# Kernel tuning notes

Hardware: AMD Instinct MI355X
Metric: run time of the kernel (lower is better)

## Reference

```python
import jax, jax.numpy as jnp
import numpy as np

B, S, D, H, MEL = 64, 512, 512, 8, 80
HD = D // H  # head dim


def _lstm_cell(x, h, c, w_ih, w_hh, b_ih, b_hh):
    # torch gate order: i, f, g, o
    gates = x @ w_ih.T + h @ w_hh.T + b_ih + b_hh
    i, f, g, o = jnp.split(gates, 4, axis=-1)
    c = jax.nn.sigmoid(f) * c + jax.nn.sigmoid(i) * jnp.tanh(g)
    h = jax.nn.sigmoid(o) * jnp.tanh(c)
    return h, c


def setup_inputs() -> dict:
    key = jax.random.key(0)
    ks = jax.random.split(key, 24)
    s = 0.05
    inp = {"encoder_output": jax.random.normal(ks[0], (B, S, D), jnp.float32)}
    # MultiheadAttention params (torch layout: in_proj [3D, D])
    inp["attn_in_w"] = jax.random.normal(ks[1], (3 * D, D), jnp.float32) * s
    inp["attn_in_b"] = jax.random.normal(ks[2], (3 * D,), jnp.float32) * s
    inp["attn_out_w"] = jax.random.normal(ks[3], (D, D), jnp.float32) * s
    inp["attn_out_b"] = jax.random.normal(ks[4], (D,), jnp.float32) * s
    # LSTM1 (2 layers)
    names = [("l1_w_ih0", (4 * D, D)), ("l1_w_hh0", (4 * D, D)), ("l1_b_ih0", (4 * D,)), ("l1_b_hh0", (4 * D,)),
             ("l1_w_ih1", (4 * D, D)), ("l1_w_hh1", (4 * D, D)), ("l1_b_ih1", (4 * D,)), ("l1_b_hh1", (4 * D,)),
             ("l2_w_ih", (4 * D, D)), ("l2_w_hh", (4 * D, D)), ("l2_b_ih", (4 * D,)), ("l2_b_hh", (4 * D,)),
             ("proj_w", (MEL, D)), ("proj_b", (MEL,))]
    for i, (n, shp) in enumerate(names):
        inp[n] = jax.random.normal(ks[5 + i], shp, jnp.float32) * s
    return inp


def reference(encoder_output, attn_in_w, attn_in_b, attn_out_w, attn_out_b,
              l1_w_ih0, l1_w_hh0, l1_b_ih0, l1_b_hh0,
              l1_w_ih1, l1_w_hh1, l1_b_ih1, l1_b_hh1,
              l2_w_ih, l2_w_hh, l2_b_ih, l2_b_hh, proj_w, proj_b):
    b, s, d = encoder_output.shape
    max_len = s * 5
    wq, wk, wv = jnp.split(attn_in_w, 3, axis=0)
    bq, bk, bv = jnp.split(attn_in_b, 3, axis=0)
    # Precompute K, V over encoder output: [B, S, H, HD]
    K = (encoder_output @ wk.T + bk).reshape(b, s, H, HD)
    V = (encoder_output @ wv.T + bv).reshape(b, s, H, HD)
    scale = 1.0 / np.sqrt(HD)

    def attend(x):  # x: [B, D] single-token query
        q = ((x @ wq.T + bq) * scale).reshape(b, H, HD)
        scores = jnp.einsum('bhd,bshd->bhs', q, K)
        w = jax.nn.softmax(scores, axis=-1)
        ctx = jnp.einsum('bhs,bshd->bhd', w, V).reshape(b, d)
        return ctx @ attn_out_w.T + attn_out_b

    zeros = jnp.zeros((b, d), encoder_output.dtype)
    carry0 = (zeros, zeros, zeros, zeros, zeros, zeros, zeros)

    def step(carry, _):
        h10, c10, h11, c11, h2, c2, dec_in = carry
        h10, c10 = _lstm_cell(dec_in, h10, c10, l1_w_ih0, l1_w_hh0, l1_b_ih0, l1_b_hh0)
        h11, c11 = _lstm_cell(h10, h11, c11, l1_w_ih1, l1_w_hh1, l1_b_ih1, l1_b_hh1)
        attn_out = attend(h11)
        h2, c2 = _lstm_cell(attn_out, h2, c2, l2_w_ih, l2_w_hh, l2_b_ih, l2_b_hh)
        out = h2 @ proj_w.T + proj_b  # [B, MEL]
        return (h10, c10, h11, c11, h2, c2, h2), out

    _, ys = jax.lax.scan(step, carry0, None, length=max_len)
    return jnp.transpose(ys, (1, 0, 2))  # [B, max_len, MEL]
```

## Files before the change

kernel.cpp:

```cpp
#include <hip/hip_runtime.h>
#include <hip/hip_bf16.h>
#include <hip/hip_fp8.h>

#define DEV_INLINE __device__ __forceinline__

typedef __attribute__((ext_vector_type(8))) short bf16x8;
typedef __attribute__((ext_vector_type(4))) float f32x4;
typedef unsigned long long ull;

constexpr int Bc = 64, Sc = 512, Dc = 512, Hc = 8, HDc = 64, MELc = 80, Tc = 2560;
constexpr int OUTSTRIDE = Tc * MELc;

constexpr size_t SZ_KP8 = 64ull * 8 * 512 * 64;
constexpr size_t SZ_VP  = 64ull * 8 * 512 * 64 * 2;
constexpr size_t SZ_PL  = 128ull * 2048 * 16;
constexpr size_t OFF_KP8 = 0;
constexpr size_t OFF_VP  = OFF_KP8 + SZ_KP8;
constexpr size_t OFF_PL0 = OFF_VP + SZ_VP;
constexpr size_t OFF_PL1 = OFF_PL0 + SZ_PL;
constexpr size_t OFF_PL2 = OFF_PL1 + SZ_PL;
constexpr size_t OFF_PWQ = OFF_PL2 + SZ_PL;
constexpr size_t OFF_PP  = OFF_PWQ + 524288;
constexpr size_t OFF_BL0 = OFF_PP + 81920;
constexpr size_t OFF_BL1 = OFF_BL0 + 8192;
constexpr size_t OFF_BL2 = OFF_BL1 + 8192;
constexpr size_t OFF_B2E = OFF_BL2 + 8192;
constexpr size_t OFF_W2E = OFF_B2E + 8192;
constexpr size_t OFF_WOT = OFF_W2E + 2097152;
constexpr size_t OFF_ACT = OFF_WOT + 1048576;
constexpr size_t OFF_FLG = OFF_ACT + 524288;

constexpr unsigned DYN_LDS = 137344;

DEV_INLINE float bf2f(short s) { return __uint_as_float(((unsigned)(unsigned short)s) << 16); }
DEV_INLINE short f2bf(float f) { union { __hip_bfloat16 h; short s; } u; u.h = __float2bfloat16(f); return u.s; }
DEV_INLINE float sig_f(float x) { return 1.0f / (1.0f + __expf(-x)); }
DEV_INLINE float tanh_f(float x) {
  float ax = fabsf(x);
  float e = __expf(fminf(2.0f * ax, 80.0f));
  float r = 1.0f - 2.0f / (e + 1.0f);
  return copysignf(r, x);
}
DEV_INLINE bf16x8 cvt8(const float* p) {
  bf16x8 r;
#pragma unroll
  for (int i = 0; i < 8; ++i) r[i] = f2bf(p[i]);
  return r;
}
DEV_INLINE float fp8tof(unsigned v) {
  __hip_fp8_e4m3 t; t.__x = (__hip_fp8_storage_t)v; return (float)t;
}

DEV_INLINE ull ld_dev_u64(const void* p) {
  return __hip_atomic_load((const ull*)p, __ATOMIC_RELAXED, __HIP_MEMORY_SCOPE_AGENT);
}
DEV_INLINE void st_dev_u64(void* p, ull v) {
  __hip_atomic_store((ull*)p, v, __ATOMIC_RELAXED, __HIP_MEMORY_SCOPE_AGENT);
}
DEV_INLINE bf16x8 ld_frag(const __hip_bfloat16* p) {
  union { bf16x8 v; ull u[2]; } r;
  r.u[0] = ld_dev_u64(p);
  r.u[1] = ld_dev_u64((const char*)p + 8);
  return r.v;
}

__global__ __launch_bounds__(256) void gemm_setup(const float* __restrict__ A,
                                                  const float* __restrict__ Bt,
                                                  const float* __restrict__ bias,
                                                  __hip_bfloat16* __restrict__ dst,
                                                  unsigned char* __restrict__ dst8,
                                                  int mode) {
  int tid = threadIdx.x, lane = tid & 63, wv = tid >> 6;
  int m0 = blockIdx.y * 64 + wv * 16;
  int nb = blockIdx.x * 64;
  int mrow = m0 + (lane & 15);
  int kb = (lane >> 4) * 8;
  f32x4 acc0 = {0,0,0,0}, acc1 = {0,0,0,0}, acc2 = {0,0,0,0}, acc3 = {0,0,0,0};
  const float* arow = A + (size_t)mrow * 512 + kb;
  const float* b0r = Bt + (size_t)(nb + 0 * 16 + (lane & 15)) * 512 + kb;
  const float* b1r = Bt + (size_t)(nb + 1 * 16 + (lane & 15)) * 512 + kb;
  const float* b2r = Bt + (size_t)(nb + 2 * 16 + (lane & 15)) * 512 + kb;
  const float* b3r = Bt + (size_t)(nb + 3 * 16 + (lane & 15)) * 512 + kb;
  for (int kk = 0; kk < 16; ++kk) {
    bf16x8 af = cvt8(arow + kk * 32);
    acc0 = __builtin_amdgcn_mfma_f32_16x16x32_bf16(af, cvt8(b0r + kk * 32), acc0, 0, 0, 0);
    acc1 = __builtin_amdgcn_mfma_f32_16x16x32_bf16(af, cvt8(b1r + kk * 32), acc1, 0, 0, 0);
    acc2 = __builtin_amdgcn_mfma_f32_16x16x32_bf16(af, cvt8(b2r + kk * 32), acc2, 0, 0, 0);
    acc3 = __builtin_amdgcn_mfma_f32_16x16x32_bf16(af, cvt8(b3r + kk * 32), acc3, 0, 0, 0);
  }
  int col16 = lane & 15, r0 = (lane >> 4) * 4;
  f32x4 accs[4] = {acc0, acc1, acc2, acc3};
#pragma unroll
  for (int nt = 0; nt < 4; ++nt) {
    int n = nb + nt * 16 + col16;
#pragma unroll
    for (int r = 0; r < 4; ++r) {
      int m = m0 + r0 + r;
      float v = accs[nt][r];
      if (mode == 0) {
        v += bias[n];
        int bb = m >> 9, s = m & 511, h = n >> 6, d = n & 63;
        dst[(((size_t)(bb * 8 + h) * 512 + s) * 64) + d] = __float2bfloat16(v);
      } else if (mode == 2) {
        v += bias[n];
        int bb = m >> 9, s = m & 511, h = n >> 6, d = n & 63;
        __hip_fp8_e4m3 q(v);
        dst8[(((size_t)(bb * 8 + h) * 512 + s) * 64) + d] = (unsigned char)q.__x;
      } else {
        dst[(size_t)m * 512 + n] = __float2bfloat16(v);
      }
    }
  }
}

__global__ __launch_bounds__(256) void transpose512(const float* __restrict__ in, float* __restrict__ out) {
  __shared__ float tl[32][33];
  int x = threadIdx.x & 31, ty = threadIdx.x >> 5;
  int bx = blockIdx.x * 32, by = blockIdx.y * 32;
#pragma unroll
  for (int r = 0; r < 4; ++r) tl[ty + r * 8][x] = in[(size_t)(by + ty + r * 8) * 512 + bx + x];
  __syncthreads();
#pragma unroll
  for (int r = 0; r < 4; ++r) out[(size_t)(bx + ty + r * 8) * 512 + by + x] = tl[x][ty + r * 8];
}

__global__ __launch_bounds__(256) void b2eff_k(const float* __restrict__ w2ih, const float* __restrict__ bout,
                                               const float* __restrict__ bih, const float* __restrict__ bhh,
                                               float* __restrict__ dst) {
  int g = blockIdx.x * 256 + threadIdx.x;
  float acc = bih[g] + bhh[g];
  const float* row = w2ih + (size_t)g * 512;
  for (int k = 0; k < 512; ++k) acc += row[k] * bout[k];
  dst[g] = acc;
}

__global__ __launch_bounds__(256) void pack_lstm(const float* __restrict__ lo_f32,
                                                 const __hip_bfloat16* __restrict__ lo_bf16,
                                                 const float* __restrict__ hi_f32,
                                                 const float* __restrict__ b1, const float* __restrict__ b2,
                                                 const float* __restrict__ b_pre,
                                                 __hip_bfloat16* __restrict__ dst, float* __restrict__ bias_out,
                                                 int mode) {
  int u = blockIdx.x, tid = threadIdx.x;
  for (int rep = 0; rep < 8; ++rep) {
    int slot = rep * 256 + tid;
    int kk = slot >> 6, lane = slot & 63;
    int n16 = lane & 15, gate = n16 >> 2, jj = n16 & 3;
    int srow = gate * 512 + u * 4 + jj;
    int k = kk * 32 + (lane >> 4) * 8;
    __hip_bfloat16 tmp[8];
    if (k < 512) {
      if (mode == 0) {
#pragma unroll
        for (int i = 0; i < 8; ++i) tmp[i] = __float2bfloat16(lo_f32[(size_t)srow * 512 + k + i]);
      } else {
#pragma unroll
        for (int i = 0; i < 8; ++i) tmp[i] = lo_bf16[(size_t)srow * 512 + k + i];
      }
    } else {
#pragma unroll
      for (int i = 0; i < 8; ++i) tmp[i] = __float2bfloat16(hi_f32[(size_t)srow * 512 + (k - 512) + i]);
    }
    *(uint4*)(dst + ((size_t)u * 2048 + slot) * 8) = *(uint4*)tmp;
  }
  if (tid < 16) {
    int gate = tid >> 2, jj = tid & 3;
    int srow = gate * 512 + u * 4 + jj;
    bias_out[u * 16 + tid] = (mode == 0) ? (b1[srow] + b2[srow]) : b_pre[srow];
  }
}

__global__ __launch_bounds__(256) void pack_wq(const float* __restrict__ wq, __hip_bfloat16* __restrict__ dst) {
  int h = blockIdx.x, tid = threadIdx.x;
  for (int rep = 0; rep < 16; ++rep) {
    int slot = rep * 256 + tid;
    int nt = slot >> 10, kk = (slot >> 6) & 15, lane = slot & 63;
    int srow = h * 64 + nt * 16 + (lane & 15);
    int k = kk * 32 + (lane >> 4) * 8;
    __hip_bfloat16 tmp[8];
#pragma unroll
    for (int i = 0; i < 8; ++i) tmp[i] = __float2bfloat16(wq[(size_t)srow * 512 + k + i]);
    *(uint4*)(dst + ((size_t)h * 4096 + slot) * 8) = *(uint4*)tmp;
  }
}

__global__ __launch_bounds__(256) void pack_proj(const float* __restrict__ pw, __hip_bfloat16* __restrict__ dst) {
  int u5 = blockIdx.x, tid = threadIdx.x;
  for (int rep = 0; rep < 4; ++rep) {
    int slot = rep * 256 + tid;
    int kk = slot >> 6, lane = slot & 63;
    int srow = u5 * 16 + (lane & 15);
    int k = kk * 32 + (lane >> 4) * 8;
    __hip_bfloat16 tmp[8];
#pragma unroll
    for (int i = 0; i < 8; ++i) tmp[i] = __float2bfloat16(pw[(size_t)srow * 512 + k + i]);
    *(uint4*)(dst + ((size_t)u5 * 1024 + slot) * 8) = *(uint4*)tmp;
  }
}

struct DecParams {
  const float* attn_in_b;
  const float* proj_b;
  const uint4* packL0; const uint4* packL1; const uint4* packL2;
  const float* biasL0; const float* biasL1; const float* biasL2;
  const uint4* packWq; const uint4* packP;
  const unsigned char* Kp8; const __hip_bfloat16* Vp;
  __hip_bfloat16* h10b; __hip_bfloat16* h11b; __hip_bfloat16* h2b; __hip_bfloat16* ctxb;
  ull* actbase;
  unsigned* flags;
  float* out;
};

constexpr ull WD_TICKS = 200000000ull;

DEV_INLINE void publish_flag(unsigned* flags, int wg, unsigned id, int tid) {
  __builtin_amdgcn_s_waitcnt(0);
  __syncthreads();
  if (tid == 0)
    __hip_atomic_store(&flags[wg], id, __ATOMIC_RELAXED, __HIP_MEMORY_SCOPE_AGENT);
}

DEV_INLINE bool wait_flags(unsigned* flags, int base, int count, unsigned id, int tid,
                           ull t0, int* bail) {
  if (tid < 64) {
    for (;;) {
      bool ok = true;
      for (int i = tid; i < count; i += 64)
        ok &= (__hip_atomic_load(&flags[base + i], __ATOMIC_RELAXED, __HIP_MEMORY_SCOPE_AGENT) >= id);
      if (__all(ok ? 1 : 0)) break;
      if (__builtin_amdgcn_s_memrealtime() - t0 > WD_TICKS) { if (tid == 0) *bail = 1; break; }
      __builtin_amdgcn_s_sleep(1);
    }
  }
  __syncthreads();
  if (*bail) return false;
  return true;
}

DEV_INLINE void prefetch_hi(bf16x8* pf, const __hip_bfloat16* hi, int g, int lane, int wv) {
  if (wv >= 2) {
    const __hip_bfloat16* p = hi + (size_t)(g * 32 + (wv & 1) * 16 + (lane & 15)) * 512 + (lane >> 4) * 8;
#pragma unroll
    for (int kk = 0; kk < 16; ++kk) pf[kk] = ld_frag(p + kk * 32);
  }
}

DEV_INLINE void lstm_stage(int tid, int g, int wgl,
                           const uint4* wlds, const float* bias,
                           const __hip_bfloat16* lo, const bf16x8* pf,
                           float* cstate, __hip_bfloat16* hc,
                           float* pred, ull* st64) {
  const int lane = tid & 63, wv = tid >> 6, mt = wv & 1, kh = wv >> 1;
  f32x4 acc = {0,0,0,0};
  if (kh == 0) {
    const __hip_bfloat16* pA = lo + (size_t)(g * 32 + mt * 16 + (lane & 15)) * 512 + (lane >> 4) * 8;
#pragma unroll
    for (int kk = 0; kk < 16; ++kk) {
      bf16x8 a = ld_frag(pA + kk * 32);
      bf16x8 b = *(const bf16x8*)(wlds + kk * 64 + lane);
      acc = __builtin_amdgcn_mfma_f32_16x16x32_bf16(a, b, acc, 0, 0, 0);
    }
  } else {
#pragma unroll
    for (int kk = 0; kk < 16; ++kk) {
      bf16x8 b = *(const bf16x8*)(wlds + (16 + kk) * 64 + lane);
      acc = __builtin_amdgcn_mfma_f32_16x16x32_bf16(pf[kk], b, acc, 0, 0, 0);
    }
  }
#pragma unroll
  for (int r = 0; r < 4; ++r) pred[wv * 256 + lane * 4 + r] = acc[r];
  __syncthreads();
  if (tid < 128) {
    int bl = tid >> 2, j = tid & 3;
    int mt2 = bl >> 4, qd = (bl & 15) >> 2, reg = bl & 3;
    const float* p0 = pred + mt2 * 256;
    const float* p1 = pred + (2 + mt2) * 256;
    int l0 = qd * 16;
    float gi = p0[(l0 + j) * 4 + reg]      + p1[(l0 + j) * 4 + reg]      + bias[j];
    float gf = p0[(l0 + 4 + j) * 4 + reg]  + p1[(l0 + 4 + j) * 4 + reg]  + bias[4 + j];
    float gg = p0[(l0 + 8 + j) * 4 + reg]  + p1[(l0 + 8 + j) * 4 + reg]  + bias[8 + j];
    float go = p0[(l0 + 12 + j) * 4 + reg] + p1[(l0 + 12 + j) * 4 + reg] + bias[12 + j];
    float c = cstate[tid & 127];
    c = sig_f(gf) * c + sig_f(gi) * tanh_f(gg);
    float h = sig_f(go) * tanh_f(c);
    cstate[tid & 127] = c;
    ((unsigned short*)st64)[tid] = (unsigned short)f2bf(h);
  }
  __syncthreads();
  if (tid < 32)
    st_dev_u64(hc + (size_t)(g * 32 + tid) * 512 + wgl * 4, st64[tid]);
}

DEV_INLINE void proj_stage(int tid, int g, int n5, const uint4* wPJ, const float* proj_b,
                           const __hip_bfloat16* h2in, float* outp, float* pred) {
  const int lane = tid & 63, wv = tid >> 6, mt = wv & 1, kh = wv >> 1;
  f32x4 acc = {0,0,0,0};
  const __hip_bfloat16* pA = h2in + (size_t)(g * 32 + mt * 16 + (lane & 15)) * 512 + kh * 256 + (lane >> 4) * 8;
#pragma unroll
  for (int kk = 0; kk < 8; ++kk) {
    bf16x8 a = ld_frag(pA + kk * 32);
    bf16x8 b = *(const bf16x8*)(wPJ + (kh * 8 + kk) * 64 + lane);
    acc = __builtin_amdgcn_mfma_f32_16x16x32_bf16(a, b, acc, 0, 0, 0);
  }
#pragma unroll
  for (int r = 0; r < 4; ++r) pred[wv * 256 + lane * 4 + r] = acc[r];
  __syncthreads();
#pragma unroll
  for (int half = 0; half < 2; ++half) {
    int gx = half * 256 + tid;
    int row = gx >> 4, col = gx & 15;
    int mt2 = row >> 4, qd = (row & 15) >> 2, reg = row & 3, ln = qd * 16 + col;
    float v = pred[mt2 * 256 + ln * 4 + reg] + pred[(2 + mt2) * 256 + ln * 4 + reg] + proj_b[n5 * 16 + col];
    outp[(size_t)(g * 32 + row) * OUTSTRIDE + n5 * 16 + col] = v;
  }
  __syncthreads();
}

__global__ __launch_bounds__(256, 1) void decoder_main(DecParams P) {
  extern __shared__ char smem[];
  uint4* wL0 = (uint4*)smem;
  uint4* wL1 = wL0 + 2048;
  uint4* wL2 = wL1 + 2048;
  uint4* wPJ = wL2 + 2048;
  ull*   st64 = (ull*)(wPJ + 1024);
  float* pred = (float*)(st64 + 32);
  float* qls  = pred + 1024;
  float* sco  = qls + 1088;
  float* red  = sco + 1024;
  float* cst  = red + 2048;
  float* smx  = cst + 384;
  float* ssum = smx + 4;
  float* sinv = ssum + 4;
  int*   sbail = (int*)(sinv + 2);

  const int wg = blockIdx.x, tid = threadIdx.x;
  const int lane = tid & 63, wv = tid >> 6;
  const int g = wg >> 7;
  const int wgl = wg & 127;
  const int fbase = g * 128;
  const int hh = wgl >> 4;
  const int b0g = (wgl & 15) * 2;
  const int bblk = b0g & ~15;

  const ull t0 = __builtin_amdgcn_s_memrealtime();

  {
    const uint4* s0 = P.packL0 + (size_t)wgl * 2048;
    const uint4* s1 = P.packL1 + (size_t)wgl * 2048;
    const uint4* s2 = P.packL2 + (size_t)wgl * 2048;
    for (int i = tid; i < 2048; i += 256) { wL0[i] = s0[i]; wL1[i] = s1[i]; wL2[i] = s2[i]; }
    if (wgl < 5) { const uint4* sp = P.packP + (size_t)wgl * 1024; for (int i = tid; i < 1024; i += 256) wPJ[i] = sp[i]; }
  }
  if (tid == 0) *sbail = 0;
  if (tid < 128) { cst[tid] = 0.0f; cst[128 + tid] = 0.0f; cst[256 + tid] = 0.0f; }
  st_dev_u64(P.actbase + (size_t)wg * 256 + tid, 0ull);
  __syncthreads();
  publish_flag(P.flags, wg, 1u, tid);
  if (!wait_flags(P.flags, 0, 256, 1u, tid, t0, sbail)) goto bail;

  for (int t = 0; t < Tc; ++t) {
    const int cur = t & 1, pv = cur ^ 1;
    const unsigned idA = 4u * t + 1, idApub = 4u * t + 2, idBpub = 4u * t + 3,
                   idCpub = 4u * t + 4, idDpub = 4u * t + 5;
    __hip_bfloat16* h10c = P.h10b + cur * 32768; __hip_bfloat16* h10p = P.h10b + pv * 32768;
    __hip_bfloat16* h11c = P.h11b + cur * 32768; __hip_bfloat16* h11p = P.h11b + pv * 32768;
    __hip_bfloat16* h2c  = P.h2b  + cur * 32768; __hip_bfloat16* h2p  = P.h2b  + pv * 32768;
    __hip_bfloat16* ctxc = P.ctxb + cur * 32768;

    {
      bf16x8 pf[16];
      prefetch_hi(pf, h10p, g, lane, wv);
      if (!wait_flags(P.flags, fbase, 128, idA, tid, t0, sbail)) goto bail;
      lstm_stage(tid, g, wgl, wL0, P.biasL0 + wgl * 16, h2p, pf, cst, h10c, pred, st64);
      publish_flag(P.flags, wg, idApub, tid);
    }
    if (wgl < 5 && t > 0)
      proj_stage(tid, g, wgl, wPJ, P.proj_b, h2p, P.out + (size_t)(t - 1) * MELc, pred);

    {
      bf16x8 pf[16];
      prefetch_hi(pf, h11p, g, lane, wv);
      if (!wait_flags(P.flags, fbase, 128, idApub, tid, t0, sbail)) goto bail;
      lstm_stage(tid, g, wgl, wL1, P.biasL1 + wgl * 16, h10c, pf, cst + 128, h11c, pred, st64);
      publish_flag(P.flags, wg, idBpub, tid);
    }

    if (!wait_flags(P.flags, fbase, 128, idBpub, tid, t0, sbail)) goto bail;
    {
      int mrow = g * 32 + bblk + (lane & 15);
      const __hip_bfloat16* pA = h11c + (size_t)mrow * 512 + (lane >> 4) * 8;
      const uint4* pB = P.packWq + (size_t)hh * 4096 + wv * 1024;
      f32x4 acc = {0,0,0,0};
#pragma unroll
      for (int kk = 0; kk < 16; ++kk) {
        bf16x8 a = ld_frag(pA + kk * 32);
        bf16x8 b = *(const bf16x8*)(pB + kk * 64 + lane);
        acc = __builtin_amdgcn_mfma_f32_16x16x32_bf16(a, b, acc, 0, 0, 0);
      }
      int col = lane & 15, row0 = (lane >> 4) << 2;
      int dg = wv * 16 + col;
      float bq = P.attn_in_b[hh * 64 + dg];
#pragma unroll
      for (int r = 0; r < 4; ++r) qls[(row0 + r) * 68 + dg] = (acc[r] + bq) * 0.125f;
    }
    __syncthreads();
    {
      int p = tid >> 7, si = tid & 127;
      int bg = g * 32 + b0g + p;
      const float* qv = qls + ((b0g & 15) + p) * 68;
      const ull* Kb = (const ull*)(P.Kp8 + (size_t)(bg * 8 + hh) * 512 * 64);
#pragma unroll
      for (int ss = 0; ss < 4; ++ss) {
        int s = si * 4 + ss;
        const ull* kr = Kb + (size_t)s * 8;
        float acc = 0.0f;
#pragma unroll
        for (int i = 0; i < 8; ++i) {
          ull kv = kr[i];
#pragma unroll
          for (int jj = 0; jj < 8; ++jj)
            acc += qv[i * 8 + jj] * fp8tof((unsigned)(kv >> (8 * jj)) & 0xFFu);
        }
        sco[p * 512 + s] = acc;
      }
    }
    __syncthreads();
    {
      int p = wv >> 1, half = wv & 1;
      int idx = tid & 127;
      float mx = -1e30f;
#pragma unroll
      for (int ss = 0; ss < 4; ++ss) mx = fmaxf(mx, sco[p * 512 + idx * 4 + ss]);
#pragma unroll
      for (int off = 32; off; off >>= 1) mx = fmaxf(mx, __shfl_xor(mx, off));
      if (lane == 0) smx[p * 2 + half] = mx;
      __syncthreads();
      float m = fmaxf(smx[p * 2], smx[p * 2 + 1]);
      float sum = 0.0f;
#pragma unroll
      for (int ss = 0; ss < 4; ++ss) {
        int ix = p * 512 + idx * 4 + ss;
        float e = __expf(sco[ix] - m);
        sco[ix] = e; sum += e;
      }
#pragma unroll
      for (int off = 32; off; off >>= 1) sum += __shfl_xor(sum, off);
      if (lane == 0) ssum[p * 2 + half] = sum;
      __syncthreads();
      if (tid < 2) sinv[tid] = 1.0f / (ssum[tid * 2] + ssum[tid * 2 + 1]);
    }
    __syncthreads();
    {
      int p = wv >> 1, half = wv & 1;
      int bg = g * 32 + b0g + p;
      int sg = lane >> 3, dj = lane & 7;
      const __hip_bfloat16* Vb = P.Vp + (size_t)(bg * 8 + hh) * 512 * 64;
      float a8[8] = {0,0,0,0,0,0,0,0};
      for (int it = 0; it < 32; ++it) {
        int s = half * 256 + it * 8 + sg;
        float w = sco[p * 512 + s];
        bf16x8 v = *(const bf16x8*)(Vb + (size_t)s * 64 + dj * 8);
#pragma unroll
        for (int e = 0; e < 8; ++e) a8[e] += w * bf2f(v[e]);
      }
      float* rp = red + ((p * 16 + half * 8 + sg) * 64) + dj * 8;
#pragma unroll
      for (int e = 0; e < 8; ++e) rp[e] = a8[e];
    }
    __syncthreads();
    if (tid < 128) {
      int p = tid >> 6, d = tid & 63;
      float sacc = 0.0f;
#pragma unroll
      for (int k = 0; k < 16; ++k) sacc += red[(p * 16 + k) * 64 + d];
      sacc *= sinv[p];
      ((unsigned short*)st64)[tid] = (unsigned short)f2bf(sacc);
    }
    __syncthreads();
    if (tid < 32) {
      int p = tid >> 4, q = tid & 15;
      st_dev_u64(ctxc + (size_t)(g * 32 + b0g + p) * 512 + hh * 64 + q * 4, st64[p * 16 + q]);
    }
    publish_flag(P.flags, wg, idCpub, tid);

    {
      bf16x8 pf[16];
      prefetch_hi(pf, h2p, g, lane, wv);
      if (!wait_flags(P.flags, fbase, 128, idCpub, tid, t0, sbail)) goto bail;
      lstm_stage(tid, g, wgl, wL2, P.biasL2 + wgl * 16, ctxc, pf, cst + 256, h2c, pred, st64);
      publish_flag(P.flags, wg, idDpub, tid);
    }
  }

  if (wgl < 5) {
    if (wait_flags(P.flags, fbase, 128, 4u * (Tc - 1) + 5, tid, t0, sbail))
      proj_stage(tid, g, wgl, wPJ, P.proj_b, P.h2b + ((Tc - 1) & 1) * 32768,
                 P.out + (size_t)(Tc - 1) * MELc, pred);
  }
  return;

bail:
  publish_flag(P.flags, wg, 0x7F000000u, tid);
}

extern "C" void kernel_launch(void* const* d_in, const int* in_sizes, int n_in,
                              void* d_out, int out_size, void* d_ws, size_t ws_size,
                              hipStream_t stream) {
  const float* enc        = (const float*)d_in[0];
  const float* attn_in_w  = (const float*)d_in[1];
  const float* attn_in_b  = (const float*)d_in[2];
  const float* attn_out_w = (const float*)d_in[3];
  const float* attn_out_b = (const float*)d_in[4];
  const float* w_ih0 = (const float*)d_in[5];
  const float* w_hh0 = (const float*)d_in[6];
  const float* b_ih0 = (const float*)d_in[7];
  const float* b_hh0 = (const float*)d_in[8];
  const float* w_ih1 = (const float*)d_in[9];
  const float* w_hh1 = (const float*)d_in[10];
  const float* b_ih1 = (const float*)d_in[11];
  const float* b_hh1 = (const float*)d_in[12];
  const float* w_ih2 = (const float*)d_in[13];
  const float* w_hh2 = (const float*)d_in[14];
  const float* b_ih2 = (const float*)d_in[15];
  const float* b_hh2 = (const float*)d_in[16];
  const float* proj_w = (const float*)d_in[17];
  const float* proj_b = (const float*)d_in[18];

  char* ws = (char*)d_ws;
  unsigned char*  Kp8 = (unsigned char*)(ws + OFF_KP8);
  __hip_bfloat16* Vp  = (__hip_bfloat16*)(ws + OFF_VP);
  __hip_bfloat16* pl0 = (__hip_bfloat16*)(ws + OFF_PL0);
  __hip_bfloat16* pl1 = (__hip_bfloat16*)(ws + OFF_PL1);
  __hip_bfloat16* pl2 = (__hip_bfloat16*)(ws + OFF_PL2);
  __hip_bfloat16* pwq = (__hip_bfloat16*)(ws + OFF_PWQ);
  __hip_bfloat16* pp  = (__hip_bfloat16*)(ws + OFF_PP);
  float* bl0 = (float*)(ws + OFF_BL0);
  float* bl1 = (float*)(ws + OFF_BL1);
  float* bl2 = (float*)(ws + OFF_BL2);
  float* b2e = (float*)(ws + OFF_B2E);
  __hip_bfloat16* w2e = (__hip_bfloat16*)(ws + OFF_W2E);
  float* wot = (float*)(ws + OFF_WOT);
  char* act  = ws + OFF_ACT;
  unsigned* flags = (unsigned*)(ws + OFF_FLG);

  hipMemsetAsync(flags, 0, 4096, stream);

  gemm_setup<<<dim3(8, 512), 256, 0, stream>>>(enc, attn_in_w + 512 * 512, attn_in_b + 512, nullptr, Kp8, 2);
  gemm_setup<<<dim3(8, 512), 256, 0, stream>>>(enc, attn_in_w + 1024 * 512, attn_in_b + 1024, Vp, nullptr, 0);
  transpose512<<<dim3(16, 16), 256, 0, stream>>>(attn_out_w, wot);
  gemm_setup<<<dim3(8, 32), 256, 0, stream>>>(w_ih2, wot, nullptr, w2e, nullptr, 1);
  b2eff_k<<<8, 256, 0, stream>>>(w_ih2, attn_out_b, b_ih2, b_hh2, b2e);
  pack_lstm<<<128, 256, 0, stream>>>(w_ih0, nullptr, w_hh0, b_ih0, b_hh0, nullptr, pl0, bl0, 0);
  pack_lstm<<<128, 256, 0, stream>>>(w_ih1, nullptr, w_hh1, b_ih1, b_hh1, nullptr, pl1, bl1, 0);
  pack_lstm<<<128, 256, 0, stream>>>(nullptr, w2e, w_hh2, nullptr, nullptr, b2e, pl2, bl2, 1);
  pack_wq<<<8, 256, 0, stream>>>(attn_in_w, pwq);
  pack_proj<<<5, 256, 0, stream>>>(proj_w, pp);

  DecParams p;
  p.attn_in_b = attn_in_b;
  p.proj_b = proj_b;
  p.packL0 = (const uint4*)pl0; p.packL1 = (const uint4*)pl1; p.packL2 = (const uint4*)pl2;
  p.biasL0 = bl0; p.biasL1 = bl1; p.biasL2 = bl2;
  p.packWq = (const uint4*)pwq; p.packP = (const uint4*)pp;
  p.Kp8 = Kp8; p.Vp = Vp;
  p.h10b = (__hip_bfloat16*)(act + 0);
  p.h11b = (__hip_bfloat16*)(act + 131072);
  p.h2b  = (__hip_bfloat16*)(act + 262144);
  p.ctxb = (__hip_bfloat16*)(act + 393216);
  p.actbase = (ull*)act;
  p.flags = flags;
  p.out = (float*)d_out;

  (void)hipFuncSetAttribute((const void*)decoder_main,
                            hipFuncAttributeMaxDynamicSharedMemorySize, DYN_LDS);
  decoder_main<<<dim3(256), dim3(256), DYN_LDS, stream>>>(p);
}
```

Baseline: 112.7 ms.

## Split flag waits into halves and vectorize fp8/bf16 attention inner loops

Replaces the block-wide wait on all 128 producer flags with per-wave waits on two 64-flag halves. The first half of the K-dimension MFMA accumulation can then start as soon as its producers publish, overlapping compute with the remaining producers. Waves that consume only prefetched data no longer block on the flags. Also rewrites the QK score loop to use packed fp8->f32 conversion builtins with vector q loads, and the PV loop to use 128-bit nontemporal loads with dual accumulators and packed f32x2 FMA. The bail handling becomes more involved, and the finer-grained synchronization relies on flag ordering matching the K-slice ownership.

```diff
diff --git a/kernel.cpp b/kernel.cpp
--- a/kernel.cpp
+++ b/kernel.cpp
@@ -6,6 +6,8 @@
 
 typedef __attribute__((ext_vector_type(8))) short bf16x8;
 typedef __attribute__((ext_vector_type(4))) float f32x4;
+typedef __attribute__((ext_vector_type(2))) float f32x2;
+typedef __attribute__((ext_vector_type(4))) unsigned int u32x4;
 typedef unsigned long long ull;
 
 constexpr int Bc = 64, Sc = 512, Dc = 512, Hc = 8, HDc = 64, MELc = 80, Tc = 2560;
@@ -49,6 +51,17 @@
 }
 DEV_INLINE float fp8tof(unsigned v) {
   __hip_fp8_e4m3 t; t.__x = (__hip_fp8_storage_t)v; return (float)t;
+}
+
+template <bool HI>
+DEV_INLINE f32x2 cvt2_fp8(unsigned w) {
+#if defined(__has_builtin) && __has_builtin(__builtin_amdgcn_cvt_pk_f32_fp8)
+  return __builtin_amdgcn_cvt_pk_f32_fp8(w, HI);
+#else
+  unsigned b = HI ? (w >> 16) : w;
+  f32x2 r; r[0] = fp8tof(b & 0xFFu); r[1] = fp8tof((b >> 8) & 0xFFu);
+  return r;
+#endif
 }
 
 DEV_INLINE ull ld_dev_u64(const void* p) {
@@ -237,6 +250,15 @@
   return true;
 }
 
+DEV_INLINE bool wait_half(unsigned* flags, int base, unsigned id, int lane, ull t0, int* sbail) {
+  for (;;) {
+    unsigned f = __hip_atomic_load(&flags[base + lane], __ATOMIC_RELAXED, __HIP_MEMORY_SCOPE_AGENT);
+    if (__all(f >= id ? 1 : 0)) return true;
+    if (__builtin_amdgcn_s_memrealtime() - t0 > WD_TICKS) { *sbail = 1; return false; }
+    __builtin_amdgcn_s_sleep(1);
+  }
+}
+
 DEV_INLINE void prefetch_hi(bf16x8* pf, const __hip_bfloat16* hi, int g, int lane, int wv) {
   if (wv >= 2) {
     const __hip_bfloat16* p = hi + (size_t)(g * 32 + (wv & 1) * 16 + (lane & 15)) * 512 + (lane >> 4) * 8;
@@ -245,20 +267,32 @@
   }
 }
 
-DEV_INLINE void lstm_stage(int tid, int g, int wgl,
+DEV_INLINE bool lstm_stage(int tid, int g, int wgl,
                            const uint4* wlds, const float* bias,
                            const __hip_bfloat16* lo, const bf16x8* pf,
                            float* cstate, __hip_bfloat16* hc,
-                           float* pred, ull* st64) {
+                           float* pred, ull* st64,
+                           unsigned* flags, int fbase, unsigned id,
+                           ull t0, int* sbail) {
   const int lane = tid & 63, wv = tid >> 6, mt = wv & 1, kh = wv >> 1;
   f32x4 acc = {0,0,0,0};
   if (kh == 0) {
     const __hip_bfloat16* pA = lo + (size_t)(g * 32 + mt * 16 + (lane & 15)) * 512 + (lane >> 4) * 8;
-#pragma unroll
-    for (int kk = 0; kk < 16; ++kk) {
-      bf16x8 a = ld_frag(pA + kk * 32);
-      bf16x8 b = *(const bf16x8*)(wlds + kk * 64 + lane);
-      acc = __builtin_amdgcn_mfma_f32_16x16x32_bf16(a, b, acc, 0, 0, 0);
+    if (wait_half(flags, fbase, id, lane, t0, sbail)) {
+#pragma unroll
+      for (int kk = 0; kk < 8; ++kk) {
+        bf16x8 a = ld_frag(pA + kk * 32);
+        bf16x8 b = *(const bf16x8*)(wlds + kk * 64 + lane);
+        acc = __builtin_amdgcn_mfma_f32_16x16x32_bf16(a, b, acc, 0, 0, 0);
+      }
+      if (wait_half(flags, fbase + 64, id, lane, t0, sbail)) {
+#pragma unroll
+        for (int kk = 8; kk < 16; ++kk) {
+          bf16x8 a = ld_frag(pA + kk * 32);
+          bf16x8 b = *(const bf16x8*)(wlds + kk * 64 + lane);
+          acc = __builtin_amdgcn_mfma_f32_16x16x32_bf16(a, b, acc, 0, 0, 0);
+        }
+      }
     }
   } else {
 #pragma unroll
@@ -270,6 +304,7 @@
 #pragma unroll
   for (int r = 0; r < 4; ++r) pred[wv * 256 + lane * 4 + r] = acc[r];
   __syncthreads();
+  if (*sbail) return false;
   if (tid < 128) {
     int bl = tid >> 2, j = tid & 3;
     int mt2 = bl >> 4, qd = (bl & 15) >> 2, reg = bl & 3;
@@ -289,6 +324,7 @@
   __syncthreads();
   if (tid < 32)
     st_dev_u64(hc + (size_t)(g * 32 + tid) * 512 + wgl * 4, st64[tid]);
+  return true;
 }
 
 DEV_INLINE void proj_stage(int tid, int g, int n5, const uint4* wPJ, const float* proj_b,
@@ -370,8 +406,8 @@
     {
       bf16x8 pf[16];
       prefetch_hi(pf, h10p, g, lane, wv);
-      if (!wait_flags(P.flags, fbase, 128, idA, tid, t0, sbail)) goto bail;
-      lstm_stage(tid, g, wgl, wL0, P.biasL0 + wgl * 16, h2p, pf, cst, h10c, pred, st64);
+      if (!lstm_stage(tid, g, wgl, wL0, P.biasL0 + wgl * 16, h2p, pf, cst, h10c, pred, st64,
+                      P.flags, fbase, idA, t0, sbail)) goto bail;
       publish_flag(P.flags, wg, idApub, tid);
     }
     if (wgl < 5 && t > 0)
@@ -380,22 +416,31 @@
     {
       bf16x8 pf[16];
       prefetch_hi(pf, h11p, g, lane, wv);
-      if (!wait_flags(P.flags, fbase, 128, idApub, tid, t0, sbail)) goto bail;
-      lstm_stage(tid, g, wgl, wL1, P.biasL1 + wgl * 16, h10c, pf, cst + 128, h11c, pred, st64);
+      if (!lstm_stage(tid, g, wgl, wL1, P.biasL1 + wgl * 16, h10c, pf, cst + 128, h11c, pred, st64,
+                      P.flags, fbase, idApub, t0, sbail)) goto bail;
       publish_flag(P.flags, wg, idBpub, tid);
     }
 
-    if (!wait_flags(P.flags, fbase, 128, idBpub, tid, t0, sbail)) goto bail;
     {
       int mrow = g * 32 + bblk + (lane & 15);
       const __hip_bfloat16* pA = h11c + (size_t)mrow * 512 + (lane >> 4) * 8;
       const uint4* pB = P.packWq + (size_t)hh * 4096 + wv * 1024;
       f32x4 acc = {0,0,0,0};
-#pragma unroll
-      for (int kk = 0; kk < 16; ++kk) {
-        bf16x8 a = ld_frag(pA + kk * 32);
-        bf16x8 b = *(const bf16x8*)(pB + kk * 64 + lane);
-        acc = __builtin_amdgcn_mfma_f32_16x16x32_bf16(a, b, acc, 0, 0, 0);
+      if (wait_half(P.flags, fbase, idBpub, lane, t0, sbail)) {
+#pragma unroll
+        for (int kk = 0; kk < 8; ++kk) {
+          bf16x8 a = ld_frag(pA + kk * 32);
+          bf16x8 b = *(const bf16x8*)(pB + kk * 64 + lane);
+          acc = __builtin_amdgcn_mfma_f32_16x16x32_bf16(a, b, acc, 0, 0, 0);
+        }
+        if (wait_half(P.flags, fbase + 64, idBpub, lane, t0, sbail)) {
+#pragma unroll
+          for (int kk = 8; kk < 16; ++kk) {
+            bf16x8 a = ld_frag(pA + kk * 32);
+            bf16x8 b = *(const bf16x8*)(pB + kk * 64 + lane);
+            acc = __builtin_amdgcn_mfma_f32_16x16x32_bf16(a, b, acc, 0, 0, 0);
+          }
+        }
       }
       int col = lane & 15, row0 = (lane >> 4) << 2;
       int dg = wv * 16 + col;
@@ -404,24 +449,33 @@
       for (int r = 0; r < 4; ++r) qls[(row0 + r) * 68 + dg] = (acc[r] + bq) * 0.125f;
     }
     __syncthreads();
+    if (*sbail) goto bail;
     {
       int p = tid >> 7, si = tid & 127;
       int bg = g * 32 + b0g + p;
       const float* qv = qls + ((b0g & 15) + p) * 68;
-      const ull* Kb = (const ull*)(P.Kp8 + (size_t)(bg * 8 + hh) * 512 * 64);
+      f32x4 q4[16];
+#pragma unroll
+      for (int i = 0; i < 16; ++i) q4[i] = *(const f32x4*)(qv + 4 * i);
+      const u32x4* Kb = (const u32x4*)(P.Kp8 + (size_t)(bg * 8 + hh) * 512 * 64);
 #pragma unroll
       for (int ss = 0; ss < 4; ++ss) {
         int s = si * 4 + ss;
-        const ull* kr = Kb + (size_t)s * 8;
-        float acc = 0.0f;
-#pragma unroll
-        for (int i = 0; i < 8; ++i) {
-          ull kv = kr[i];
-#pragma unroll
-          for (int jj = 0; jj < 8; ++jj)
-            acc += qv[i * 8 + jj] * fp8tof((unsigned)(kv >> (8 * jj)) & 0xFFu);
+        const u32x4* kr = Kb + s * 4;
+        f32x2 acc2 = {0.0f, 0.0f};
+#pragma unroll
+        for (int i = 0; i < 4; ++i) {
+          u32x4 kv = kr[i];
+#pragma unroll
+          for (int j = 0; j < 4; ++j) {
+            unsigned w = kv[j];
+            f32x2 c01 = cvt2_fp8<false>(w);
+            f32x2 c23 = cvt2_fp8<true>(w);
+            f32x4 qq = q4[i * 4 + j];
+            acc2 += c01 * (f32x2){qq[0], qq[1]} + c23 * (f32x2){qq[2], qq[3]};
+          }
         }
-        sco[p * 512 + s] = acc;
+        sco[p * 512 + s] = acc2[0] + acc2[1];
       }
     }
     __syncthreads();
@@ -454,18 +508,32 @@
       int p = wv >> 1, half = wv & 1;
       int bg = g * 32 + b0g + p;
       int sg = lane >> 3, dj = lane & 7;
-      const __hip_bfloat16* Vb = P.Vp + (size_t)(bg * 8 + hh) * 512 * 64;
-      float a8[8] = {0,0,0,0,0,0,0,0};
-      for (int it = 0; it < 32; ++it) {
-        int s = half * 256 + it * 8 + sg;
-        float w = sco[p * 512 + s];
-        bf16x8 v = *(const bf16x8*)(Vb + (size_t)s * 64 + dj * 8);
-#pragma unroll
-        for (int e = 0; e < 8; ++e) a8[e] += w * bf2f(v[e]);
+      const u32x4* VbU = (const u32x4*)(P.Vp + (size_t)(bg * 8 + hh) * 512 * 64);
+      f32x2 aA[4] = {{0,0},{0,0},{0,0},{0,0}};
+      f32x2 aB[4] = {{0,0},{0,0},{0,0},{0,0}};
+      const int s0 = half * 256 + sg;
+#pragma unroll 4
+      for (int it = 0; it < 16; ++it) {
+        int sA = s0 + it * 8, sB = sA + 128;
+        u32x4 vA = __builtin_nontemporal_load(VbU + (size_t)sA * 8 + dj);
+        u32x4 vB = __builtin_nontemporal_load(VbU + (size_t)sB * 8 + dj);
+        float wa = sco[p * 512 + sA], wb = sco[p * 512 + sB];
+        f32x2 wA = {wa, wa}, wB = {wb, wb};
+#pragma unroll
+        for (int j = 0; j < 4; ++j) {
+          unsigned ua = vA[j], ub = vB[j];
+          f32x2 fa = { __uint_as_float(ua << 16), __uint_as_float(ua & 0xFFFF0000u) };
+          f32x2 fb = { __uint_as_float(ub << 16), __uint_as_float(ub & 0xFFFF0000u) };
+          aA[j] += wA * fa;
+          aB[j] += wB * fb;
+        }
       }
       float* rp = red + ((p * 16 + half * 8 + sg) * 64) + dj * 8;
 #pragma unroll
-      for (int e = 0; e < 8; ++e) rp[e] = a8[e];
+      for (int j = 0; j < 4; ++j) {
+        rp[j * 2]     = aA[j][0] + aB[j][0];
+        rp[j * 2 + 1] = aA[j][1] + aB[j][1];
+      }
     }
     __syncthreads();
     if (tid < 128) {
@@ -486,8 +554,8 @@
     {
       bf16x8 pf[16];
       prefetch_hi(pf, h2p, g, lane, wv);
-      if (!wait_flags(P.flags, fbase, 128, idCpub, tid, t0, sbail)) goto bail;
-      lstm_stage(tid, g, wgl, wL2, P.biasL2 + wgl * 16, ctxc, pf, cst + 256, h2c, pred, st64);
+      if (!lstm_stage(tid, g, wgl, wL2, P.biasL2 + wgl * 16, ctxc, pf, cst + 256, h2c, pred, st64,
+                      P.flags, fbase, idCpub, t0, sbail)) goto bail;
       publish_flag(P.flags, wg, idDpub, tid);
     }
   }
```

Measured after the change: 111.6 ms. No clear change (-0.9%).
